# Kernel optimization log

Hardware: AMD Instinct MI355X
Metric: run time of the kernel (lower is better)

## Reference

```python
import jax, jax.numpy as jnp
import numpy as np

INPUT_DIM = 1024
HIDDEN_DIM = 1024
FORGET_BIAS = 0.0


def setup_inputs() -> dict:
    key = jax.random.key(0)
    ks = jax.random.split(key, 8)
    x = jax.random.normal(ks[0], (1024, 32, INPUT_DIM), dtype=jnp.float32)
    state = jnp.zeros((1, 32, HIDDEN_DIM), dtype=jnp.float32)
    std = 0.1
    wm_z = std * jax.random.normal(ks[1], (HIDDEN_DIM, INPUT_DIM), dtype=jnp.float32)
    wm_f = std * jax.random.normal(ks[2], (HIDDEN_DIM, INPUT_DIM), dtype=jnp.float32)
    wv_z = std * jax.random.normal(ks[3], (1, HIDDEN_DIM), dtype=jnp.float32)
    wv_f = std * jax.random.normal(ks[4], (1, HIDDEN_DIM), dtype=jnp.float32)
    bias_z = std * jax.random.normal(ks[5], (1, HIDDEN_DIM), dtype=jnp.float32)
    bias_f = std * jax.random.normal(ks[6], (1, HIDDEN_DIM), dtype=jnp.float32) + FORGET_BIAS
    return {"x": x, "state": state, "wm_z": wm_z, "wm_f": wm_f,
            "wv_z": wv_z, "wv_f": wv_f, "bias_z": bias_z, "bias_f": bias_f}


def reference(x, state, wm_z, wm_f, wv_z, wv_f, bias_z, bias_f):
    # x: [slen, bsz, in_dim]; state: [1, bsz, hidden]
    hidden_prev = state[0]  # [bsz, hidden]
    # Pre-activation input projections (batched GEMM over all timesteps).
    out_z = jnp.einsum('sbi,hi->sbh', x, wm_z)  # [slen, bsz, hidden]
    out_f = jnp.einsum('sbi,hi->sbh', x, wm_f)

    def step(cell, zf):
        z_, f_ = zf
        z_part = jnp.tanh(z_ + wv_z * cell + bias_z)
        f_part = jax.nn.sigmoid(f_ + wv_f * cell + bias_f)
        new_cell = cell * f_part + (1.0 - f_part) * z_part
        return new_cell, new_cell

    _, new_cells = jax.lax.scan(step, hidden_prev, (out_z, out_f))
    return new_cells  # [slen, bsz, hidden]
```

## Files before the change

### kernel.cpp

```cpp
#include <hip/hip_runtime.h>
#include <hip/hip_fp16.h>

#define S_LEN 1024
#define BSZ   32
#define IN_DIM 1024
#define HID   1024
#define MDIM  (S_LEN*BSZ)
#define NDIM  (2*HID)
#define KDIM  IN_DIM

typedef __attribute__((ext_vector_type(8))) _Float16 half8;
typedef __attribute__((ext_vector_type(2))) _Float16 half2v;
typedef __attribute__((ext_vector_type(4))) float    floatx4;

__global__ void cvt_x_kernel(const float* __restrict__ x, _Float16* __restrict__ xh) {
    int idx = blockIdx.x * blockDim.x + threadIdx.x;
    const float4* src = (const float4*)x + (size_t)idx * 2;
    float4 a = src[0], b = src[1];
    half8 h;
    h[0] = (_Float16)a.x; h[1] = (_Float16)a.y; h[2] = (_Float16)a.z; h[3] = (_Float16)a.w;
    h[4] = (_Float16)b.x; h[5] = (_Float16)b.y; h[6] = (_Float16)b.z; h[7] = (_Float16)b.w;
    *((half8*)xh + idx) = h;
}

__global__ void cvt_w_kernel(const float* __restrict__ wz, const float* __restrict__ wf,
                             _Float16* __restrict__ wh) {
    int idx = blockIdx.x * blockDim.x + threadIdx.x;
    int e0 = idx * 8;
    int r   = e0 >> 10;
    int col = e0 & 1023;
    int g = r >> 5, sub = r & 31;
    const float* src = (sub < 16)
        ? wz + ((size_t)(g * 16 + sub)      * KDIM + col)
        : wf + ((size_t)(g * 16 + sub - 16) * KDIM + col);
    const float4* s4 = (const float4*)src;
    float4 a = s4[0], b = s4[1];
    half8 h;
    h[0] = (_Float16)a.x; h[1] = (_Float16)a.y; h[2] = (_Float16)a.z; h[3] = (_Float16)a.w;
    h[4] = (_Float16)b.x; h[5] = (_Float16)b.y; h[6] = (_Float16)b.z; h[7] = (_Float16)b.w;
    *((half8*)wh + idx) = h;
}

#define BM 256
#define BN 256
#define BK 64
#define NKT (KDIM / BK)
#define NIT (NKT / 2)

__global__ __launch_bounds__(512, 2) void gemm_f16_kernel(
    const _Float16* __restrict__ A, const _Float16* __restrict__ B,
    uint* __restrict__ zf) {
    __shared__ __attribute__((aligned(128))) _Float16 smem[65536];
    char* smb = (char*)smem;

    const int tid  = threadIdx.x;
    const int lane = tid & 63;
    const int wv   = tid >> 6;
    const int wm_off = (wv >> 2) * 128;
    const int wn_off = (wv & 3) * 64;

    const int flat   = blockIdx.x;
    const int xcd    = flat & 7;
    const int local  = flat >> 3;
    const int tile_m = (local >> 3) * 8 + xcd;
    const int tile_n = local & 7;
    const int m0  = tile_m * BM;
    const int n0g = tile_n * BN;

    const int fr  = lane & 15;
    const int fkb = (lane >> 4) * 16;

    const int srow = lane >> 3;
    const int skb  = ((lane & 7) ^ srow) << 4;

    floatx4 acc[8][4] = {};

    auto STAGE = [&](const _Float16* __restrict__ src, int gRow0, int regionBase,
                     int R0, int kt) {
        int r = R0 + wv * 8 + srow;
        const _Float16* gp = src + (size_t)(gRow0 + r) * KDIM + kt * BK + (skb >> 1);
        __builtin_amdgcn_global_load_lds(
            (const __attribute__((address_space(1))) void*)gp,
            (__attribute__((address_space(3))) void*)(smb + regionBase + (R0 + wv * 8) * 128),
            16, 0, 0);
    };
    auto LD8 = [&](int rb, int r, int kb) -> half8 {
        return *(const half8*)(smb + rb + r * 128 + (kb ^ ((r & 7) << 4)));
    };

    STAGE(B, n0g, 32768, 0, 0);           STAGE(B, n0g, 32768, 64, 0);
    STAGE(A, m0, 0, 0, 0);                STAGE(A, m0, 0, 128, 0);
    STAGE(B, n0g, 32768, 128, 0);         STAGE(B, n0g, 32768, 192, 0);
    STAGE(A, m0, 0, 64, 0);               STAGE(A, m0, 0, 192, 0);
    STAGE(B, n0g, 65536 + 32768, 0, 1);   STAGE(B, n0g, 65536 + 32768, 64, 1);
    STAGE(A, m0, 65536, 0, 1);            STAGE(A, m0, 65536, 128, 1);
    STAGE(B, n0g, 65536 + 32768, 128, 1); STAGE(B, n0g, 65536 + 32768, 192, 1);
    asm volatile("s_waitcnt vmcnt(6)" ::: "memory");
    __builtin_amdgcn_s_barrier();
    asm volatile("" ::: "memory");

    half8 bfr[4][2];
    for (int it = 0; it < NIT; ++it) {
        const int  t    = 2 * it;
        const bool more = (it < NIT - 1);
        #pragma unroll
        for (int ph = 0; ph < 8; ++ph) {
            const int bb    = ph >> 2;
            const int p     = ph & 3;
            const int bbase = bb * 65536;

            if (p == 0) {
                #pragma unroll
                for (int j = 0; j < 4; ++j)
                    #pragma unroll
                    for (int ks = 0; ks < 2; ++ks) {
                        int r = wn_off + j * 16 + fr;
                        bfr[j][ks] = LD8(bbase + 32768, r, ks * 64 + fkb);
                    }
            }
            half8 afr[2][2];
            #pragma unroll
            for (int ii = 0; ii < 2; ++ii)
                #pragma unroll
                for (int ks = 0; ks < 2; ++ks) {
                    int r = wm_off + (2 * p + ii) * 16 + fr;
                    afr[ii][ks] = LD8(bbase, r, ks * 64 + fkb);
                }

            if (ph == 0) {
                STAGE(A, m0, 65536, 64, t + 1);  STAGE(A, m0, 65536, 192, t + 1);
            } else if (more) {
                if      (ph == 1) { STAGE(B, n0g, 32768, 0, t + 2);          STAGE(B, n0g, 32768, 64, t + 2); }
                else if (ph == 2) { STAGE(A, m0, 0, 0, t + 2);               STAGE(A, m0, 0, 128, t + 2); }
                else if (ph == 3) { STAGE(B, n0g, 32768, 128, t + 2);        STAGE(B, n0g, 32768, 192, t + 2); }
                else if (ph == 4) { STAGE(A, m0, 0, 64, t + 2);              STAGE(A, m0, 0, 192, t + 2); }
                else if (ph == 5) { STAGE(B, n0g, 65536 + 32768, 0, t + 3);  STAGE(B, n0g, 65536 + 32768, 64, t + 3); }
                else if (ph == 6) { STAGE(A, m0, 65536, 0, t + 3);           STAGE(A, m0, 65536, 128, t + 3); }
                else              { STAGE(B, n0g, 65536 + 32768, 128, t + 3); STAGE(B, n0g, 65536 + 32768, 192, t + 3); }
            }

            __builtin_amdgcn_s_barrier();
            asm volatile("s_waitcnt lgkmcnt(0)" ::: "memory");
            __builtin_amdgcn_s_setprio(1);
            #pragma unroll
            for (int ks = 0; ks < 2; ++ks)
                #pragma unroll
                for (int ii = 0; ii < 2; ++ii)
                    #pragma unroll
                    for (int j = 0; j < 4; ++j)
                        acc[2 * p + ii][j] = __builtin_amdgcn_mfma_f32_16x16x32_f16(
                            afr[ii][ks], bfr[j][ks], acc[2 * p + ii][j], 0, 0, 0);
            __builtin_amdgcn_s_setprio(0);
            if (ph == 3) {
                if (more) asm volatile("s_waitcnt vmcnt(6)" ::: "memory");
                else      asm volatile("s_waitcnt vmcnt(0)" ::: "memory");
            } else if (ph == 7) {
                if (more) asm volatile("s_waitcnt vmcnt(6)" ::: "memory");
            }
            __builtin_amdgcn_s_barrier();
            asm volatile("" ::: "memory");
        }
    }

    const int orow = (lane >> 4) * 4;
    const int ocol = lane & 15;
    const int gb   = (n0g + wn_off) >> 5;
    #pragma unroll
    for (int i = 0; i < 8; ++i)
        #pragma unroll
        for (int p2 = 0; p2 < 2; ++p2) {
            int hh = (gb + p2) * 16 + ocol;
            #pragma unroll
            for (int r = 0; r < 4; ++r) {
                int row = m0 + wm_off + i * 16 + orow + r;
                half2v v;
                v[0] = (_Float16)acc[i][2 * p2][r];
                v[1] = (_Float16)acc[i][2 * p2 + 1][r];
                *(half2v*)(zf + (size_t)row * HID + hh) = v;
            }
        }
}

#define UNR 32
__global__ __launch_bounds__(64) void scan_kernel(
    const uint* __restrict__ zf, float* __restrict__ out,
    const float* __restrict__ state,
    const float* __restrict__ wvz, const float* __restrict__ wvf,
    const float* __restrict__ bz, const float* __restrict__ bfv) {
    const int t = blockIdx.x * 64 + threadIdx.x;
    const int h = t & (HID - 1);
    const int stride = BSZ * HID;

    float cell = state[t];
    const float az = wvz[h], afc = wvf[h], cz = bz[h], cf = bfv[h];

    const uint* p = zf + t;
    float* po = out + t;

    uint buf[UNR];
    #pragma unroll
    for (int u = 0; u < UNR; ++u) buf[u] = p[(size_t)u * stride];

    for (int s0 = 0; s0 < S_LEN; s0 += UNR) {
        uint nb[UNR];
        if (s0 + UNR < S_LEN) {
            #pragma unroll
            for (int u = 0; u < UNR; ++u)
                nb[u] = p[(size_t)(s0 + UNR + u) * stride];
        }
        #pragma unroll
        for (int u = 0; u < UNR; ++u) {
            half2v h2 = __builtin_bit_cast(half2v, buf[u]);
            float zpre = (float)h2[0] + az * cell + cz;
            float fpre = (float)h2[1] + afc * cell + cf;
            float ez = __expf(2.0f * zpre);
            float zp = (ez - 1.0f) * __builtin_amdgcn_rcpf(ez + 1.0f);
            float fp = __builtin_amdgcn_rcpf(1.0f + __expf(-fpre));
            cell = fmaf(cell - zp, fp, zp);
            po[(size_t)(s0 + u) * stride] = cell;
        }
        #pragma unroll
        for (int u = 0; u < UNR; ++u) buf[u] = nb[u];
    }
}

extern "C" void kernel_launch(void* const* d_in, const int* in_sizes, int n_in,
                              void* d_out, int out_size, void* d_ws, size_t ws_size,
                              hipStream_t stream) {
    const float* x      = (const float*)d_in[0];
    const float* state  = (const float*)d_in[1];
    const float* wm_z   = (const float*)d_in[2];
    const float* wm_f   = (const float*)d_in[3];
    const float* wv_z   = (const float*)d_in[4];
    const float* wv_f   = (const float*)d_in[5];
    const float* bias_z = (const float*)d_in[6];
    const float* bias_f = (const float*)d_in[7];
    float* out = (float*)d_out;

    char* ws = (char*)d_ws;
    _Float16* xh = (_Float16*)ws;
    _Float16* wh = (_Float16*)(ws + (size_t)MDIM * KDIM * sizeof(_Float16));
    uint* zf     = (uint*)(ws + (size_t)MDIM * KDIM * sizeof(_Float16)
                              + (size_t)NDIM * KDIM * sizeof(_Float16));

    cvt_x_kernel<<<(MDIM * KDIM) / (256 * 8), 256, 0, stream>>>(x, xh);
    cvt_w_kernel<<<(NDIM * KDIM) / (256 * 8), 256, 0, stream>>>(wm_z, wm_f, wh);

    gemm_f16_kernel<<<(MDIM / BM) * (NDIM / BN), 512, 0, stream>>>(xh, wh, zf);

    scan_kernel<<<MDIM / 64, 64, 0, stream>>>(zf, out, state, wv_z, wv_f, bias_z, bias_f);
}
```

Measured before the change: 436.6 us.

## Make GEMM persistent over four M tiles per block and streamline scan exp math

```diff
diff --git a/kernel.cpp b/kernel.cpp
--- a/kernel.cpp
+++ b/kernel.cpp
@@ -44,8 +44,9 @@
 #define BM 256
 #define BN 256
 #define BK 64
-#define NKT (KDIM / BK)
-#define NIT (NKT / 2)
+#define TPB 4
+#define NGT (TPB * 16)
+#define NIT (NGT / 2)
 
 __global__ __launch_bounds__(512, 2) void gemm_f16_kernel(
     const _Float16* __restrict__ A, const _Float16* __restrict__ B,
@@ -59,13 +60,8 @@
     const int wm_off = (wv >> 2) * 128;
     const int wn_off = (wv & 3) * 64;
 
-    const int flat   = blockIdx.x;
-    const int xcd    = flat & 7;
-    const int local  = flat >> 3;
-    const int tile_m = (local >> 3) * 8 + xcd;
-    const int tile_n = local & 7;
-    const int m0  = tile_m * BM;
-    const int n0g = tile_n * BN;
+    const int n0g  = (blockIdx.x & 7) * BN;
+    const int m_bs = (blockIdx.x >> 3) * (TPB * BM);
 
     const int fr  = lane & 15;
     const int fkb = (lane >> 4) * 16;
@@ -75,26 +71,35 @@
 
     floatx4 acc[8][4] = {};
 
-    auto STAGE = [&](const _Float16* __restrict__ src, int gRow0, int regionBase,
-                     int R0, int kt) {
+    auto STAGE_A = [&](int g, int R0) {
+        int kt = g & 15, mt = (g >> 4) & 3;
         int r = R0 + wv * 8 + srow;
-        const _Float16* gp = src + (size_t)(gRow0 + r) * KDIM + kt * BK + (skb >> 1);
+        const _Float16* gp = A + (size_t)(m_bs + mt * BM + r) * KDIM + kt * BK + (skb >> 1);
         __builtin_amdgcn_global_load_lds(
             (const __attribute__((address_space(1))) void*)gp,
-            (__attribute__((address_space(3))) void*)(smb + regionBase + (R0 + wv * 8) * 128),
+            (__attribute__((address_space(3))) void*)(smb + (g & 1) * 65536 + (R0 + wv * 8) * 128),
+            16, 0, 0);
+    };
+    auto STAGE_B = [&](int g, int R0) {
+        int kt = g & 15;
+        int r = R0 + wv * 8 + srow;
+        const _Float16* gp = B + (size_t)(n0g + r) * KDIM + kt * BK + (skb >> 1);
+        __builtin_amdgcn_global_load_lds(
+            (const __attribute__((address_space(1))) void*)gp,
+            (__attribute__((address_space(3))) void*)(smb + (g & 1) * 65536 + 32768 + (R0 + wv * 8) * 128),
             16, 0, 0);
     };
     auto LD8 = [&](int rb, int r, int kb) -> half8 {
         return *(const half8*)(smb + rb + r * 128 + (kb ^ ((r & 7) << 4)));
     };
 
-    STAGE(B, n0g, 32768, 0, 0);           STAGE(B, n0g, 32768, 64, 0);
-    STAGE(A, m0, 0, 0, 0);                STAGE(A, m0, 0, 128, 0);
-    STAGE(B, n0g, 32768, 128, 0);         STAGE(B, n0g, 32768, 192, 0);
-    STAGE(A, m0, 0, 64, 0);               STAGE(A, m0, 0, 192, 0);
-    STAGE(B, n0g, 65536 + 32768, 0, 1);   STAGE(B, n0g, 65536 + 32768, 64, 1);
-    STAGE(A, m0, 65536, 0, 1);            STAGE(A, m0, 65536, 128, 1);
-    STAGE(B, n0g, 65536 + 32768, 128, 1); STAGE(B, n0g, 65536 + 32768, 192, 1);
+    STAGE_B(0, 0);   STAGE_B(0, 64);
+    STAGE_A(0, 0);   STAGE_A(0, 128);
+    STAGE_B(0, 128); STAGE_B(0, 192);
+    STAGE_A(0, 64);  STAGE_A(0, 192);
+    STAGE_B(1, 0);   STAGE_B(1, 64);
+    STAGE_A(1, 0);   STAGE_A(1, 128);
+    STAGE_B(1, 128); STAGE_B(1, 192);
     asm volatile("s_waitcnt vmcnt(6)" ::: "memory");
     __builtin_amdgcn_s_barrier();
     asm volatile("" ::: "memory");
@@ -128,15 +133,15 @@
                 }
 
             if (ph == 0) {
-                STAGE(A, m0, 65536, 64, t + 1);  STAGE(A, m0, 65536, 192, t + 1);
+                STAGE_A(t + 1, 64);  STAGE_A(t + 1, 192);
             } else if (more) {
-                if      (ph == 1) { STAGE(B, n0g, 32768, 0, t + 2);          STAGE(B, n0g, 32768, 64, t + 2); }
-                else if (ph == 2) { STAGE(A, m0, 0, 0, t + 2);               STAGE(A, m0, 0, 128, t + 2); }
-                else if (ph == 3) { STAGE(B, n0g, 32768, 128, t + 2);        STAGE(B, n0g, 32768, 192, t + 2); }
-                else if (ph == 4) { STAGE(A, m0, 0, 64, t + 2);              STAGE(A, m0, 0, 192, t + 2); }
-                else if (ph == 5) { STAGE(B, n0g, 65536 + 32768, 0, t + 3);  STAGE(B, n0g, 65536 + 32768, 64, t + 3); }
-                else if (ph == 6) { STAGE(A, m0, 65536, 0, t + 3);           STAGE(A, m0, 65536, 128, t + 3); }
-                else              { STAGE(B, n0g, 65536 + 32768, 128, t + 3); STAGE(B, n0g, 65536 + 32768, 192, t + 3); }
+                if      (ph == 1) { STAGE_B(t + 2, 0);   STAGE_B(t + 2, 64);  }
+                else if (ph == 2) { STAGE_A(t + 2, 0);   STAGE_A(t + 2, 128); }
+                else if (ph == 3) { STAGE_B(t + 2, 128); STAGE_B(t + 2, 192); }
+                else if (ph == 4) { STAGE_A(t + 2, 64);  STAGE_A(t + 2, 192); }
+                else if (ph == 5) { STAGE_B(t + 3, 0);   STAGE_B(t + 3, 64);  }
+                else if (ph == 6) { STAGE_A(t + 3, 0);   STAGE_A(t + 3, 128); }
+                else              { STAGE_B(t + 3, 128); STAGE_B(t + 3, 192); }
             }
 
             __builtin_amdgcn_s_barrier();
@@ -160,28 +165,41 @@
             __builtin_amdgcn_s_barrier();
             asm volatile("" ::: "memory");
         }
+
+        if ((it & 7) == 7) {
+            const int m0   = m_bs + (it >> 3) * BM;
+            const int orow = (lane >> 4) * 4;
+            const int ocol = lane & 15;
+            const int gb   = (n0g + wn_off) >> 5;
+            #pragma unroll
+            for (int i = 0; i < 8; ++i)
+                #pragma unroll
+                for (int p2 = 0; p2 < 2; ++p2) {
+                    int hh = (gb + p2) * 16 + ocol;
+                    #pragma unroll
+                    for (int r = 0; r < 4; ++r) {
+                        int row = m0 + wm_off + i * 16 + orow + r;
+                        half2v v;
+                        v[0] = (_Float16)acc[i][2 * p2][r];
+                        v[1] = (_Float16)acc[i][2 * p2 + 1][r];
+                        *(half2v*)(zf + (size_t)row * HID + hh) = v;
+                    }
+                }
+            #pragma unroll
+            for (int i = 0; i < 8; ++i)
+                #pragma unroll
+                for (int j = 0; j < 4; ++j)
+                    acc[i][j] = (floatx4)0.0f;
+        }
     }
-
-    const int orow = (lane >> 4) * 4;
-    const int ocol = lane & 15;
-    const int gb   = (n0g + wn_off) >> 5;
-    #pragma unroll
-    for (int i = 0; i < 8; ++i)
-        #pragma unroll
-        for (int p2 = 0; p2 < 2; ++p2) {
-            int hh = (gb + p2) * 16 + ocol;
-            #pragma unroll
-            for (int r = 0; r < 4; ++r) {
-                int row = m0 + wm_off + i * 16 + orow + r;
-                half2v v;
-                v[0] = (_Float16)acc[i][2 * p2][r];
-                v[1] = (_Float16)acc[i][2 * p2 + 1][r];
-                *(half2v*)(zf + (size_t)row * HID + hh) = v;
-            }
-        }
 }
 
 #define UNR 32
+__device__ __forceinline__ float fast_exp2(float x) {
+    float r;
+    asm("v_exp_f32 %0, %1" : "=v"(r) : "v"(x));
+    return r;
+}
 __global__ __launch_bounds__(64) void scan_kernel(
     const uint* __restrict__ zf, float* __restrict__ out,
     const float* __restrict__ state,
@@ -192,7 +210,11 @@
     const int stride = BSZ * HID;
 
     float cell = state[t];
-    const float az = wvz[h], afc = wvf[h], cz = bz[h], cf = bfv[h];
+    const float L2E = 1.44269504088896f;
+    const float azt = 2.0f * L2E * wvz[h];
+    const float czt = 2.0f * L2E * bz[h];
+    const float aft = -L2E * wvf[h];
+    const float cft = -L2E * bfv[h];
 
     const uint* p = zf + t;
     float* po = out + t;
@@ -211,11 +233,12 @@
         #pragma unroll
         for (int u = 0; u < UNR; ++u) {
             half2v h2 = __builtin_bit_cast(half2v, buf[u]);
-            float zpre = (float)h2[0] + az * cell + cz;
-            float fpre = (float)h2[1] + afc * cell + cf;
-            float ez = __expf(2.0f * zpre);
-            float zp = (ez - 1.0f) * __builtin_amdgcn_rcpf(ez + 1.0f);
-            float fp = __builtin_amdgcn_rcpf(1.0f + __expf(-fpre));
+            float zb = fmaf((float)h2[0], 2.0f * L2E, czt);
+            float fb = fmaf((float)h2[1], -L2E, cft);
+            float ez = fast_exp2(fmaf(azt, cell, zb));
+            float zp = fmaf(-2.0f, __builtin_amdgcn_rcpf(ez + 1.0f), 1.0f);
+            float ef = fast_exp2(fmaf(aft, cell, fb));
+            float fp = __builtin_amdgcn_rcpf(ef + 1.0f);
             cell = fmaf(cell - zp, fp, zp);
             po[(size_t)(s0 + u) * stride] = cell;
         }
@@ -246,7 +269,7 @@
     cvt_x_kernel<<<(MDIM * KDIM) / (256 * 8), 256, 0, stream>>>(x, xh);
     cvt_w_kernel<<<(NDIM * KDIM) / (256 * 8), 256, 0, stream>>>(wm_z, wm_f, wh);
 
-    gemm_f16_kernel<<<(MDIM / BM) * (NDIM / BN), 512, 0, stream>>>(xh, wh, zf);
+    gemm_f16_kernel<<<256, 512, 0, stream>>>(xh, wh, zf);
 
     scan_kernel<<<MDIM / 64, 64, 0, stream>>>(zf, out, state, wv_z, wv_f, bias_z, bias_f);
 }
```

Result: faster. 425.1 us (-2.6%).
